# Kernel optimization log

Measured on AMD Instinct MI355X. Metric: run time of the kernel, lower is better.

## Reference

```python
import jax, jax.numpy as jnp
import numpy as np

N_HARM_XYZ = 6
N_HARM_DIR = 4
HIDDEN_XYZ = 256
HIDDEN_DIR = 128
EMB_XYZ = N_HARM_XYZ * 2 * 3 + 3  # 39
EMB_DIR = N_HARM_DIR * 2 * 3 + 3  # 27


def harmonic_embedding(x, n_harmonics):
    # x: [..., 3] -> [..., n_harmonics*2*3 + 3]
    freqs = 2.0 ** jnp.arange(n_harmonics, dtype=x.dtype)  # logspace, omega0=1
    emb = (x[..., None] * freqs).reshape(*x.shape[:-1], -1)  # [..., 3*n_harm]
    return jnp.concatenate([jnp.sin(emb), jnp.cos(emb), x], axis=-1)


def setup_inputs() -> dict:
    key = jax.random.key(0)
    ks = jax.random.split(key, 32)
    R, P = 2048, 64
    inp = {
        'sample_points': jax.random.normal(ks[0], (R, P, 3), dtype=jnp.float32),
        'directions': jax.random.normal(ks[1], (R, 3), dtype=jnp.float32),
    }
    # trunk layer dims (skip concat before layer 5; last layer outputs hidden+1)
    dims_in = [EMB_XYZ, HIDDEN_XYZ, HIDDEN_XYZ, HIDDEN_XYZ, HIDDEN_XYZ,
               HIDDEN_XYZ + EMB_XYZ, HIDDEN_XYZ, HIDDEN_XYZ]
    dims_out = [HIDDEN_XYZ] * 7 + [HIDDEN_XYZ + 1]
    for i, (di, do) in enumerate(zip(dims_in, dims_out)):
        s = 1.0 / np.sqrt(di)
        inp[f'W{i}'] = jax.random.uniform(ks[2 + 2 * i], (di, do), jnp.float32, -s, s)
        inp[f'b{i}'] = jax.random.uniform(ks[3 + 2 * i], (do,), jnp.float32, -s, s)
    s = 1.0 / np.sqrt(HIDDEN_XYZ + EMB_DIR)
    inp['Wc'] = jax.random.uniform(ks[20], (HIDDEN_XYZ + EMB_DIR, HIDDEN_DIR), jnp.float32, -s, s)
    inp['bc'] = jax.random.uniform(ks[21], (HIDDEN_DIR,), jnp.float32, -s, s)
    s = 1.0 / np.sqrt(HIDDEN_DIR)
    inp['Wo'] = jax.random.uniform(ks[22], (HIDDEN_DIR, 3), jnp.float32, -s, s)
    inp['bo'] = jax.random.uniform(ks[23], (3,), jnp.float32, -s, s)
    return inp


def nerf_forward(sample_points, directions,
                 W0, b0, W1, b1, W2, b2, W3, b3, W4, b4, W5, b5, W6, b6, W7, b7,
                 Wc, bc, Wo, bo):
    R, P, _ = sample_points.shape
    pts = sample_points.reshape(-1, 3)              # [N, 3]
    e = harmonic_embedding(pts, N_HARM_XYZ)         # [N, 39]
    h = e
    # seq0: layers 0-4, ReLU after each
    for W, b in ((W0, b0), (W1, b1), (W2, b2), (W3, b3), (W4, b4)):
        h = jax.nn.relu(h @ W + b)
    # skip concat with xyz embedding, then seq1: layers 5-7 (no ReLU after last)
    h = jnp.concatenate([h, e], axis=-1)            # [N, 295]
    h = jax.nn.relu(h @ W5 + b5)
    h = jax.nn.relu(h @ W6 + b6)
    h = h @ W7 + b7                                  # [N, 257]
    sigma = jax.nn.relu(h[:, 0]).reshape(R, P, 1)
    dirs = jnp.broadcast_to(directions[:, None, :], (R, P, 3)).reshape(-1, 3)
    d = harmonic_embedding(dirs, N_HARM_DIR)         # [N, 27]
    c = jnp.concatenate([h[:, 1:], d], axis=-1)      # [N, 283]
    c = jax.nn.relu(c @ Wc + bc)
    color = jax.nn.sigmoid(c @ Wo + bo).reshape(R, P, 3)
    return color, sigma


def reference(sample_points, directions,
              W0, b0, W1, b1, W2, b2, W3, b3, W4, b4, W5, b5, W6, b6, W7, b7,
              Wc, bc, Wo, bo):
    # returns (feature, density) matching the torch dict values
    return nerf_forward(sample_points, directions,
                        W0, b0, W1, b1, W2, b2, W3, b3, W4, b4, W5, b5, W6, b6, W7, b7,
                        Wc, bc, Wo, bo)
```

## Files before the change

kernel.cpp:

```cpp
#include <hip/hip_runtime.h>

typedef __attribute__((ext_vector_type(8))) __bf16 bf16x8;
typedef __attribute__((ext_vector_type(4))) float float4_;
typedef __attribute__((ext_vector_type(4))) unsigned short ushort4_;
typedef __attribute__((ext_vector_type(8))) unsigned short ushort8_;

#define OFF_W0T 0
#define OFF_W1T 16384
#define OFF_W2T 81920
#define OFF_W3T 147456
#define OFF_W4T 212992
#define OFF_W5T 278528
#define OFF_W6T 360448
#define OFF_W7T 425984
#define OFF_WCT 491520
#define BF16_TOTAL 524288
#define WSF_BYTE_OFF (BF16_TOTAL * 2)

__device__ __forceinline__ unsigned short f2b(float v) {
  union { float f; unsigned u; } a; a.f = v;
  unsigned r = a.u + 0x7fffu + ((a.u >> 16) & 1u);
  return (unsigned short)(r >> 16);
}

__device__ __forceinline__ ushort4_ pack4(float4_ v) {
#if __has_builtin(__builtin_amdgcn_cvt_pk_bf16_f32)
  auto p0 = __builtin_amdgcn_cvt_pk_bf16_f32(v.x, v.y);
  auto p1 = __builtin_amdgcn_cvt_pk_bf16_f32(v.z, v.w);
  union { decltype(p0) p; unsigned u; } u0, u1;
  u0.p = p0; u1.p = p1;
  ushort4_ r;
  r.x = (unsigned short)(u0.u & 0xffffu); r.y = (unsigned short)(u0.u >> 16);
  r.z = (unsigned short)(u1.u & 0xffffu); r.w = (unsigned short)(u1.u >> 16);
  return r;
#else
  ushort4_ r; r.x = f2b(v.x); r.y = f2b(v.y); r.z = f2b(v.z); r.w = f2b(v.w);
  return r;
#endif
}

__global__ __launch_bounds__(256) void prep_kernel(
    const float* __restrict__ W0, const float* __restrict__ W1,
    const float* __restrict__ W2, const float* __restrict__ W3,
    const float* __restrict__ W4, const float* __restrict__ W5,
    const float* __restrict__ W6, const float* __restrict__ W7,
    const float* __restrict__ Wc, const float* __restrict__ b7,
    unsigned short* __restrict__ wsb, float* __restrict__ wsf)
{
  int i = blockIdx.x * 256 + threadIdx.x;
  const float* src; int rs, K, n, k2, nt16; unsigned short* base;
  if (i < 8192)        { int t = i;          n = t & 255; k2 = t >> 8; src = W0; rs = 256; K = 39;  nt16 = 16; base = wsb + OFF_W0T; }
  else if (i < 139264) { int t = i - 8192;   int l = t >> 15; t &= 32767;
                         n = t & 255; k2 = t >> 8;
                         src = (l == 0) ? W1 : (l == 1) ? W2 : (l == 2) ? W3 : W4;
                         rs = 256; K = 256; nt16 = 16; base = wsb + OFF_W1T + l * 65536; }
  else if (i < 180224) { int t = i - 139264; n = t & 255; k2 = t >> 8; src = W5;     rs = 256; K = 295; nt16 = 16; base = wsb + OFF_W5T; }
  else if (i < 212992) { int t = i - 180224; n = t & 255; k2 = t >> 8; src = W6;     rs = 256; K = 256; nt16 = 16; base = wsb + OFF_W6T; }
  else if (i < 245760) { int t = i - 212992; n = t & 255; k2 = t >> 8; src = W7 + 1; rs = 257; K = 256; nt16 = 16; base = wsb + OFF_W7T; }
  else if (i < 262144) { int t = i - 245760; n = t & 127; k2 = t >> 7; src = Wc;     rs = 128; K = 256; nt16 = 8;  base = wsb + OFF_WCT; }
  else if (i < 262400) { int k = i - 262144; wsf[k] = W7[k * 257]; return; }
  else if (i < 262656) { int k = i - 262400; wsf[256 + k] = b7[k + 1]; return; }
  else return;
  const int k = k2 * 2;
  const float v0 = (k     < K) ? src[k * rs + n]       : 0.f;
  const float v1 = (k + 1 < K) ? src[(k + 1) * rs + n] : 0.f;
  const int off = ((k >> 5) * nt16 + (n >> 4)) * 512
                + ((k >> 3) & 3) * 128 + (n & 15) * 8 + (k & 7);
  const unsigned val = (unsigned)f2b(v0) | ((unsigned)f2b(v1) << 16);
  *(unsigned*)(base + off) = val;
}

template<int NT, int NTB, int KS1, int KS2, bool RELU>
__device__ __forceinline__ void layer_mm(
    const unsigned short* src1, const unsigned short* src2,
    const unsigned short* __restrict__ wT,
    const float* bias, unsigned short* dst, int lane, int wave)
{
  constexpr int KT = KS1 + KS2;
  const int c = lane & 15, q = lane >> 4;
  const int n0 = wave * (NT * 16);
  const unsigned short* wl = wT + (wave * NT) * 512 + lane * 8;

  float4_ acc[4][NT];
#pragma unroll
  for (int ni = 0; ni < NT; ++ni) {
    float4_ bv = *(const float4_*)(bias + n0 + ni * 16 + q * 4);
#pragma unroll
    for (int mi = 0; mi < 4; ++mi) acc[mi][ni] = bv;
  }

  bf16x8 aC[NT], aN[NT];
#pragma unroll
  for (int ni = 0; ni < NT; ++ni)
    aC[ni] = *(const bf16x8*)(wl + ni * 512);
#pragma unroll
  for (int ks = 0; ks < KT; ++ks) {
    if (ks + 1 < KT) {
#pragma unroll
      for (int ni = 0; ni < NT; ++ni)
        aN[ni] = *(const bf16x8*)(wl + ((ks + 1) * NTB + ni) * 512);
    }
    const unsigned short* bsrc = (ks < KS1) ? src1 + (ks * 4) * 512
                                            : src2 + ((ks - KS1) * 4) * 512;
    bf16x8 bfr[4];
#pragma unroll
    for (int mi = 0; mi < 4; ++mi)
      bfr[mi] = *(const bf16x8*)(bsrc + mi * 512 + lane * 8);
#pragma unroll
    for (int ni = 0; ni < NT; ++ni)
#pragma unroll
      for (int mi = 0; mi < 4; ++mi)
        acc[mi][ni] = __builtin_amdgcn_mfma_f32_16x16x32_bf16(aC[ni], bfr[mi], acc[mi][ni], 0, 0, 0);
    if (ks + 1 < KT) {
#pragma unroll
      for (int ni = 0; ni < NT; ++ni) aC[ni] = aN[ni];
    }
  }
#pragma unroll
  for (int ni = 0; ni < NT; ++ni) {
    const int base = n0 + ni * 16 + q * 4;
#pragma unroll
    for (int mi = 0; mi < 4; ++mi) {
      float4_ v = acc[mi][ni];
      if (RELU) {
        v.x = fmaxf(v.x, 0.f); v.y = fmaxf(v.y, 0.f);
        v.z = fmaxf(v.z, 0.f); v.w = fmaxf(v.w, 0.f);
      }
      const int addr = ((base >> 5) * 4 + mi) * 512
                     + ((base >> 3) & 3) * 128 + c * 8 + (base & 7);
      *(ushort4_*)(dst + addr) = pack4(v);
    }
  }
}

__global__ __launch_bounds__(256, 2) void nerf_kernel(
    const float* __restrict__ pts, const float* __restrict__ dirs,
    const float* __restrict__ b0, const float* __restrict__ b1,
    const float* __restrict__ b2, const float* __restrict__ b3,
    const float* __restrict__ b4, const float* __restrict__ b5,
    const float* __restrict__ b6, const float* __restrict__ b7,
    const float* __restrict__ Wc, const float* __restrict__ bc,
    const float* __restrict__ Wo, const float* __restrict__ bo,
    const unsigned short* __restrict__ wsb, const float* __restrict__ wsf,
    float* __restrict__ out)
{
  __shared__ __align__(16) unsigned short sA[32 * 512];
  __shared__ __align__(16) unsigned short sB[40 * 512];
  __shared__ float s_dvec[27];
  __shared__ float s_biasc[128];

  const int ray = blockIdx.x;
  const int t = threadIdx.x;
  const int lane = t & 63;
  const int wave = t >> 6;
  unsigned short* sE = sB + 32 * 512;

  {
    const int m = t >> 2, s4 = t & 3;
    const float* pb = pts + (ray * 64 + m) * 3;
    const float x0 = pb[0], x1 = pb[1], x2 = pb[2];
#pragma unroll
    for (int h = 0; h < 2; ++h) {
      ushort8_ ev;
#pragma unroll
      for (int j = 0; j < 8; ++j) {
        const int cc = s4 * 16 + h * 8 + j;
        float v = 0.f;
        if (cc < 18) {
          const float xx = (cc < 6) ? x0 : (cc < 12) ? x1 : x2;
          v = sinf(xx * (float)(1 << (cc % 6)));
        } else if (cc < 36) {
          const int c2 = cc - 18;
          const float xx = (c2 < 6) ? x0 : (c2 < 12) ? x1 : x2;
          v = cosf(xx * (float)(1 << (c2 % 6)));
        } else if (cc == 36) v = x0;
        else if (cc == 37) v = x1;
        else if (cc == 38) v = x2;
        ev[j] = f2b(v);
      }
      const int cc0 = s4 * 16 + h * 8;
      *(ushort8_*)(sE + ((cc0 >> 5) * 4 + (m >> 4)) * 512
                      + ((cc0 >> 3) & 3) * 128 + (m & 15) * 8) = ev;
    }
  }
  if (t < 27) {
    const float* db = dirs + ray * 3;
    float v;
    if (t < 12) v = sinf(db[t >> 2] * (float)(1 << (t & 3)));
    else if (t < 24) { const int j = t - 12; v = cosf(db[j >> 2] * (float)(1 << (j & 3))); }
    else v = db[t - 24];
    s_dvec[t] = v;
  }
  __syncthreads();
  if (t < 128) {
    float s = bc[t];
#pragma unroll
    for (int j = 0; j < 27; ++j) s += s_dvec[j] * Wc[(256 + j) * 128 + t];
    s_biasc[t] = s;
  }

  layer_mm<4, 16, 2,  0, true >(sE, nullptr, wsb + OFF_W0T, b0, sA, lane, wave); __syncthreads();
  layer_mm<4, 16, 8,  0, true >(sA, nullptr, wsb + OFF_W1T, b1, sB, lane, wave); __syncthreads();
  layer_mm<4, 16, 8,  0, true >(sB, nullptr, wsb + OFF_W2T, b2, sA, lane, wave); __syncthreads();
  layer_mm<4, 16, 8,  0, true >(sA, nullptr, wsb + OFF_W3T, b3, sB, lane, wave); __syncthreads();
  layer_mm<4, 16, 8,  0, true >(sB, nullptr, wsb + OFF_W4T, b4, sA, lane, wave); __syncthreads();
  layer_mm<4, 16, 8,  2, true >(sA, sE,      wsb + OFF_W5T, b5, sB, lane, wave); __syncthreads();
  layer_mm<4, 16, 8,  0, true >(sB, nullptr, wsb + OFF_W6T, b6, sA, lane, wave); __syncthreads();

  {
    const int m = t >> 2, q4 = t & 3;
    float s = 0.f;
#pragma unroll
    for (int i8 = 0; i8 < 8; ++i8) {
      const int kb = q4 * 64 + i8 * 8;
      bf16x8 hv = *(const bf16x8*)(sA + ((kb >> 5) * 4 + (m >> 4)) * 512
                                      + ((kb >> 3) & 3) * 128 + (m & 15) * 8);
      const float* w = wsf + kb;
#pragma unroll
      for (int j = 0; j < 8; ++j) s += (float)hv[j] * w[j];
    }
    s += __shfl_xor(s, 1); s += __shfl_xor(s, 2);
    if (q4 == 0) out[393216 + ray * 64 + m] = fmaxf(s + b7[0], 0.f);
  }

  layer_mm<4, 16, 8, 0, false>(sA, nullptr, wsb + OFF_W7T, wsf + 256, sB, lane, wave); __syncthreads();
  layer_mm<2, 8,  8, 0, true >(sB, nullptr, wsb + OFF_WCT, s_biasc, sA, lane, wave); __syncthreads();

  {
    const int m = t >> 2, q4 = t & 3;
    float s0 = 0.f, s1 = 0.f, s2 = 0.f;
#pragma unroll
    for (int i8 = 0; i8 < 4; ++i8) {
      const int kb = q4 * 32 + i8 * 8;
      bf16x8 cv = *(const bf16x8*)(sA + ((kb >> 5) * 4 + (m >> 4)) * 512
                                      + ((kb >> 3) & 3) * 128 + (m & 15) * 8);
#pragma unroll
      for (int j = 0; j < 8; ++j) {
        const float cc = (float)cv[j];
        const float* w = Wo + (kb + j) * 3;
        s0 += cc * w[0]; s1 += cc * w[1]; s2 += cc * w[2];
      }
    }
    s0 += __shfl_xor(s0, 1); s0 += __shfl_xor(s0, 2);
    s1 += __shfl_xor(s1, 1); s1 += __shfl_xor(s1, 2);
    s2 += __shfl_xor(s2, 1); s2 += __shfl_xor(s2, 2);
    if (q4 == 0) {
      float* oc = out + (ray * 64 + m) * 3;
      oc[0] = 1.f / (1.f + __expf(-(s0 + bo[0])));
      oc[1] = 1.f / (1.f + __expf(-(s1 + bo[1])));
      oc[2] = 1.f / (1.f + __expf(-(s2 + bo[2])));
    }
  }
}

extern "C" void kernel_launch(void* const* d_in, const int* in_sizes, int n_in,
                              void* d_out, int out_size, void* d_ws, size_t ws_size,
                              hipStream_t stream)
{
  const float* pts  = (const float*)d_in[0];
  const float* dirs = (const float*)d_in[1];
  const float* W0 = (const float*)d_in[2];   const float* b0 = (const float*)d_in[3];
  const float* W1 = (const float*)d_in[4];   const float* b1 = (const float*)d_in[5];
  const float* W2 = (const float*)d_in[6];   const float* b2 = (const float*)d_in[7];
  const float* W3 = (const float*)d_in[8];   const float* b3 = (const float*)d_in[9];
  const float* W4 = (const float*)d_in[10];  const float* b4 = (const float*)d_in[11];
  const float* W5 = (const float*)d_in[12];  const float* b5 = (const float*)d_in[13];
  const float* W6 = (const float*)d_in[14];  const float* b6 = (const float*)d_in[15];
  const float* W7 = (const float*)d_in[16];  const float* b7 = (const float*)d_in[17];
  const float* Wc = (const float*)d_in[18];  const float* bc = (const float*)d_in[19];
  const float* Wo = (const float*)d_in[20];  const float* bo = (const float*)d_in[21];

  unsigned short* wsb = (unsigned short*)d_ws;
  float* wsf = (float*)((char*)d_ws + WSF_BYTE_OFF);

  prep_kernel<<<1026, 256, 0, stream>>>(W0, W1, W2, W3, W4, W5, W6, W7, Wc, b7, wsb, wsf);
  nerf_kernel<<<2048, 256, 0, stream>>>(pts, dirs, b0, b1, b2, b3, b4, b5, b6, b7,
                                        Wc, bc, Wo, bo, wsb, wsf, (float*)d_out);
}
```

Measured before the change: 287.1 us.

## Process two rays per 512-thread block to double weight reuse per MFMA

Each block now handles 128 sample points (two rays) with 8 waves. Each wave covers 8 M-tiles and half as many N-tiles, so every weight fragment loaded from global memory feeds twice as many MFMAs, halving weight traffic per point. Activations are updated in place in one LDS buffer guarded by barriers inside the layer routine. The xyz embedding is stored row-major with the tail K-slice zero-masked, and the per-ray colour bias is split into two halves. The cost is more accumulator registers, extra barriers per layer, and a larger LDS footprint per block.

```diff
diff --git a/kernel.cpp b/kernel.cpp
--- a/kernel.cpp
+++ b/kernel.cpp
@@ -21,6 +21,13 @@
   union { float f; unsigned u; } a; a.f = v;
   unsigned r = a.u + 0x7fffu + ((a.u >> 16) & 1u);
   return (unsigned short)(r >> 16);
+}
+
+__device__ __forceinline__ bf16x8 bzero() {
+  union { ushort8_ u; bf16x8 b; } z;
+  ushort8_ t = {0, 0, 0, 0, 0, 0, 0, 0};
+  z.u = t;
+  return z.b;
 }
 
 __device__ __forceinline__ ushort4_ pack4(float4_ v) {
@@ -70,29 +77,31 @@
   *(unsigned*)(base + off) = val;
 }
 
-template<int NT, int NTB, int KS1, int KS2, bool RELU>
+template<int NT, int NTB, int KS1, int KSE, bool RELU>
 __device__ __forceinline__ void layer_mm(
-    const unsigned short* src1, const unsigned short* src2,
+    const unsigned short* sAct, const unsigned short* sEmb,
     const unsigned short* __restrict__ wT,
-    const float* bias, unsigned short* dst, int lane, int wave)
-{
-  constexpr int KT = KS1 + KS2;
+    const float* bias0, const float* bias1,
+    unsigned short* dst, int lane, int wave)
+{
+  constexpr int KT = KS1 + KSE;
   const int c = lane & 15, q = lane >> 4;
   const int n0 = wave * (NT * 16);
   const unsigned short* wl = wT + (wave * NT) * 512 + lane * 8;
 
-  float4_ acc[4][NT];
+  float4_ acc[8][NT];
 #pragma unroll
   for (int ni = 0; ni < NT; ++ni) {
-    float4_ bv = *(const float4_*)(bias + n0 + ni * 16 + q * 4);
-#pragma unroll
-    for (int mi = 0; mi < 4; ++mi) acc[mi][ni] = bv;
+    float4_ bv0 = *(const float4_*)(bias0 + n0 + ni * 16 + q * 4);
+    float4_ bv1 = *(const float4_*)(bias1 + n0 + ni * 16 + q * 4);
+#pragma unroll
+    for (int mi = 0; mi < 8; ++mi) acc[mi][ni] = (mi < 4) ? bv0 : bv1;
   }
 
   bf16x8 aC[NT], aN[NT];
 #pragma unroll
-  for (int ni = 0; ni < NT; ++ni)
-    aC[ni] = *(const bf16x8*)(wl + ni * 512);
+  for (int ni = 0; ni < NT; ++ni) aC[ni] = *(const bf16x8*)(wl + ni * 512);
+
 #pragma unroll
   for (int ks = 0; ks < KT; ++ks) {
     if (ks + 1 < KT) {
@@ -100,40 +109,53 @@
       for (int ni = 0; ni < NT; ++ni)
         aN[ni] = *(const bf16x8*)(wl + ((ks + 1) * NTB + ni) * 512);
     }
-    const unsigned short* bsrc = (ks < KS1) ? src1 + (ks * 4) * 512
-                                            : src2 + ((ks - KS1) * 4) * 512;
-    bf16x8 bfr[4];
-#pragma unroll
-    for (int mi = 0; mi < 4; ++mi)
-      bfr[mi] = *(const bf16x8*)(bsrc + mi * 512 + lane * 8);
-#pragma unroll
-    for (int ni = 0; ni < NT; ++ni)
-#pragma unroll
-      for (int mi = 0; mi < 4; ++mi)
-        acc[mi][ni] = __builtin_amdgcn_mfma_f32_16x16x32_bf16(aC[ni], bfr[mi], acc[mi][ni], 0, 0, 0);
+#pragma unroll
+    for (int mh = 0; mh < 2; ++mh) {
+      bf16x8 bfr[4];
+#pragma unroll
+      for (int m4 = 0; m4 < 4; ++m4) {
+        const int mi = mh * 4 + m4;
+        if (ks < KS1) {
+          bfr[m4] = *(const bf16x8*)(sAct + (ks * 8 + mi) * 512 + lane * 8);
+        } else {
+          const int kse = ks - KS1;
+          bf16x8 ev = *(const bf16x8*)(sEmb + (mi * 16 + c) * 40 + kse * 32 + q * 8);
+          bfr[m4] = (kse == 0 || q == 0) ? ev : bzero();
+        }
+      }
+#pragma unroll
+      for (int ni = 0; ni < NT; ++ni)
+#pragma unroll
+        for (int m4 = 0; m4 < 4; ++m4)
+          acc[mh * 4 + m4][ni] = __builtin_amdgcn_mfma_f32_16x16x32_bf16(
+              aC[ni], bfr[m4], acc[mh * 4 + m4][ni], 0, 0, 0);
+    }
     if (ks + 1 < KT) {
 #pragma unroll
       for (int ni = 0; ni < NT; ++ni) aC[ni] = aN[ni];
     }
   }
+
+  __syncthreads();
 #pragma unroll
   for (int ni = 0; ni < NT; ++ni) {
     const int base = n0 + ni * 16 + q * 4;
 #pragma unroll
-    for (int mi = 0; mi < 4; ++mi) {
+    for (int mi = 0; mi < 8; ++mi) {
       float4_ v = acc[mi][ni];
       if (RELU) {
         v.x = fmaxf(v.x, 0.f); v.y = fmaxf(v.y, 0.f);
         v.z = fmaxf(v.z, 0.f); v.w = fmaxf(v.w, 0.f);
       }
-      const int addr = ((base >> 5) * 4 + mi) * 512
+      const int addr = ((base >> 5) * 8 + mi) * 512
                      + ((base >> 3) & 3) * 128 + c * 8 + (base & 7);
       *(ushort4_*)(dst + addr) = pack4(v);
     }
   }
-}
-
-__global__ __launch_bounds__(256, 2) void nerf_kernel(
+  __syncthreads();
+}
+
+__global__ __launch_bounds__(512, 4) void nerf_kernel(
     const float* __restrict__ pts, const float* __restrict__ dirs,
     const float* __restrict__ b0, const float* __restrict__ b1,
     const float* __restrict__ b2, const float* __restrict__ b3,
@@ -144,68 +166,63 @@
     const unsigned short* __restrict__ wsb, const float* __restrict__ wsf,
     float* __restrict__ out)
 {
-  __shared__ __align__(16) unsigned short sA[32 * 512];
-  __shared__ __align__(16) unsigned short sB[40 * 512];
-  __shared__ float s_dvec[27];
-  __shared__ float s_biasc[128];
-
-  const int ray = blockIdx.x;
+  __shared__ __align__(16) unsigned short sAct[64 * 512];
+  __shared__ __align__(16) unsigned short sEmb[128 * 40 + 64];
+  __shared__ float s_dvec[54];
+  __shared__ float s_biasc[256];
+
+  const int blk = blockIdx.x;
   const int t = threadIdx.x;
   const int lane = t & 63;
   const int wave = t >> 6;
-  unsigned short* sE = sB + 32 * 512;
 
   {
     const int m = t >> 2, s4 = t & 3;
-    const float* pb = pts + (ray * 64 + m) * 3;
+    const float* pb = pts + (blk * 128 + m) * 3;
     const float x0 = pb[0], x1 = pb[1], x2 = pb[2];
 #pragma unroll
-    for (int h = 0; h < 2; ++h) {
-      ushort8_ ev;
-#pragma unroll
-      for (int j = 0; j < 8; ++j) {
-        const int cc = s4 * 16 + h * 8 + j;
-        float v = 0.f;
-        if (cc < 18) {
-          const float xx = (cc < 6) ? x0 : (cc < 12) ? x1 : x2;
-          v = sinf(xx * (float)(1 << (cc % 6)));
-        } else if (cc < 36) {
-          const int c2 = cc - 18;
-          const float xx = (c2 < 6) ? x0 : (c2 < 12) ? x1 : x2;
-          v = cosf(xx * (float)(1 << (c2 % 6)));
-        } else if (cc == 36) v = x0;
-        else if (cc == 37) v = x1;
-        else if (cc == 38) v = x2;
-        ev[j] = f2b(v);
-      }
-      const int cc0 = s4 * 16 + h * 8;
-      *(ushort8_*)(sE + ((cc0 >> 5) * 4 + (m >> 4)) * 512
-                      + ((cc0 >> 3) & 3) * 128 + (m & 15) * 8) = ev;
-    }
-  }
-  if (t < 27) {
-    const float* db = dirs + ray * 3;
+    for (int j = 0; j < 10; ++j) {
+      const int cc = s4 * 10 + j;
+      float v = 0.f;
+      if (cc < 18) {
+        const float xx = (cc < 6) ? x0 : (cc < 12) ? x1 : x2;
+        v = sinf(xx * (float)(1 << (cc % 6)));
+      } else if (cc < 36) {
+        const int c2 = cc - 18;
+        const float xx = (c2 < 6) ? x0 : (c2 < 12) ? x1 : x2;
+        v = cosf(xx * (float)(1 << (c2 % 6)));
+      } else if (cc == 36) v = x0;
+      else if (cc == 37) v = x1;
+      else if (cc == 38) v = x2;
+      sEmb[m * 40 + cc] = f2b(v);
+    }
+  }
+  if (t < 54) {
+    const int r = (t >= 27) ? 1 : 0;
+    const int j = t - r * 27;
+    const float* db = dirs + (blk * 2 + r) * 3;
     float v;
-    if (t < 12) v = sinf(db[t >> 2] * (float)(1 << (t & 3)));
-    else if (t < 24) { const int j = t - 12; v = cosf(db[j >> 2] * (float)(1 << (j & 3))); }
-    else v = db[t - 24];
+    if (j < 12) v = sinf(db[j >> 2] * (float)(1 << (j & 3)));
+    else if (j < 24) { const int j2 = j - 12; v = cosf(db[j2 >> 2] * (float)(1 << (j2 & 3))); }
+    else v = db[j - 24];
     s_dvec[t] = v;
   }
   __syncthreads();
-  if (t < 128) {
-    float s = bc[t];
-#pragma unroll
-    for (int j = 0; j < 27; ++j) s += s_dvec[j] * Wc[(256 + j) * 128 + t];
+  if (t < 256) {
+    const int r = t >> 7, n = t & 127;
+    float s = bc[n];
+#pragma unroll
+    for (int j = 0; j < 27; ++j) s += s_dvec[r * 27 + j] * Wc[(256 + j) * 128 + n];
     s_biasc[t] = s;
   }
 
-  layer_mm<4, 16, 2,  0, true >(sE, nullptr, wsb + OFF_W0T, b0, sA, lane, wave); __syncthreads();
-  layer_mm<4, 16, 8,  0, true >(sA, nullptr, wsb + OFF_W1T, b1, sB, lane, wave); __syncthreads();
-  layer_mm<4, 16, 8,  0, true >(sB, nullptr, wsb + OFF_W2T, b2, sA, lane, wave); __syncthreads();
-  layer_mm<4, 16, 8,  0, true >(sA, nullptr, wsb + OFF_W3T, b3, sB, lane, wave); __syncthreads();
-  layer_mm<4, 16, 8,  0, true >(sB, nullptr, wsb + OFF_W4T, b4, sA, lane, wave); __syncthreads();
-  layer_mm<4, 16, 8,  2, true >(sA, sE,      wsb + OFF_W5T, b5, sB, lane, wave); __syncthreads();
-  layer_mm<4, 16, 8,  0, true >(sB, nullptr, wsb + OFF_W6T, b6, sA, lane, wave); __syncthreads();
+  layer_mm<2, 16, 0, 2, true >(sAct, sEmb, wsb + OFF_W0T, b0, b0, sAct, lane, wave);
+  layer_mm<2, 16, 8, 0, true >(sAct, sEmb, wsb + OFF_W1T, b1, b1, sAct, lane, wave);
+  layer_mm<2, 16, 8, 0, true >(sAct, sEmb, wsb + OFF_W2T, b2, b2, sAct, lane, wave);
+  layer_mm<2, 16, 8, 0, true >(sAct, sEmb, wsb + OFF_W3T, b3, b3, sAct, lane, wave);
+  layer_mm<2, 16, 8, 0, true >(sAct, sEmb, wsb + OFF_W4T, b4, b4, sAct, lane, wave);
+  layer_mm<2, 16, 8, 2, true >(sAct, sEmb, wsb + OFF_W5T, b5, b5, sAct, lane, wave);
+  layer_mm<2, 16, 8, 0, true >(sAct, sEmb, wsb + OFF_W6T, b6, b6, sAct, lane, wave);
 
   {
     const int m = t >> 2, q4 = t & 3;
@@ -213,18 +230,18 @@
 #pragma unroll
     for (int i8 = 0; i8 < 8; ++i8) {
       const int kb = q4 * 64 + i8 * 8;
-      bf16x8 hv = *(const bf16x8*)(sA + ((kb >> 5) * 4 + (m >> 4)) * 512
-                                      + ((kb >> 3) & 3) * 128 + (m & 15) * 8);
+      bf16x8 hv = *(const bf16x8*)(sAct + ((kb >> 5) * 8 + (m >> 4)) * 512
+                                       + ((kb >> 3) & 3) * 128 + (m & 15) * 8);
       const float* w = wsf + kb;
 #pragma unroll
       for (int j = 0; j < 8; ++j) s += (float)hv[j] * w[j];
     }
     s += __shfl_xor(s, 1); s += __shfl_xor(s, 2);
-    if (q4 == 0) out[393216 + ray * 64 + m] = fmaxf(s + b7[0], 0.f);
-  }
-
-  layer_mm<4, 16, 8, 0, false>(sA, nullptr, wsb + OFF_W7T, wsf + 256, sB, lane, wave); __syncthreads();
-  layer_mm<2, 8,  8, 0, true >(sB, nullptr, wsb + OFF_WCT, s_biasc, sA, lane, wave); __syncthreads();
+    if (q4 == 0) out[393216 + blk * 128 + m] = fmaxf(s + b7[0], 0.f);
+  }
+
+  layer_mm<2, 16, 8, 0, false>(sAct, sEmb, wsb + OFF_W7T, wsf + 256, wsf + 256, sAct, lane, wave);
+  layer_mm<1, 8,  8, 0, true >(sAct, sEmb, wsb + OFF_WCT, s_biasc, s_biasc + 128, sAct, lane, wave);
 
   {
     const int m = t >> 2, q4 = t & 3;
@@ -232,8 +249,8 @@
 #pragma unroll
     for (int i8 = 0; i8 < 4; ++i8) {
       const int kb = q4 * 32 + i8 * 8;
-      bf16x8 cv = *(const bf16x8*)(sA + ((kb >> 5) * 4 + (m >> 4)) * 512
-                                      + ((kb >> 3) & 3) * 128 + (m & 15) * 8);
+      bf16x8 cv = *(const bf16x8*)(sAct + ((kb >> 5) * 8 + (m >> 4)) * 512
+                                       + ((kb >> 3) & 3) * 128 + (m & 15) * 8);
 #pragma unroll
       for (int j = 0; j < 8; ++j) {
         const float cc = (float)cv[j];
@@ -245,7 +262,7 @@
     s1 += __shfl_xor(s1, 1); s1 += __shfl_xor(s1, 2);
     s2 += __shfl_xor(s2, 1); s2 += __shfl_xor(s2, 2);
     if (q4 == 0) {
-      float* oc = out + (ray * 64 + m) * 3;
+      float* oc = out + (blk * 128 + m) * 3;
       oc[0] = 1.f / (1.f + __expf(-(s0 + bo[0])));
       oc[1] = 1.f / (1.f + __expf(-(s1 + bo[1])));
       oc[2] = 1.f / (1.f + __expf(-(s2 + bo[2])));
@@ -274,6 +291,6 @@
   float* wsf = (float*)((char*)d_ws + WSF_BYTE_OFF);
 
   prep_kernel<<<1026, 256, 0, stream>>>(W0, W1, W2, W3, W4, W5, W6, W7, Wc, b7, wsb, wsf);
-  nerf_kernel<<<2048, 256, 0, stream>>>(pts, dirs, b0, b1, b2, b3, b4, b5, b6, b7,
+  nerf_kernel<<<1024, 512, 0, stream>>>(pts, dirs, b0, b1, b2, b3, b4, b5, b6, b7,
                                         Wc, bc, Wo, bo, wsb, wsf, (float*)d_out);
 }
```

After: 241.0 us. 16.1% less time.
